# Kernel optimization log

Hardware: AMD Instinct MI355X
Metric: run time of the kernel (lower is better)

Reference implementation:

```python
import jax, jax.numpy as jnp
import numpy as np

S = 4096      # sequence length == contextlen
D_IN = 1024   # input_size
E = 512       # embed_dim = input_size // 2 (divisor=2)
OUT = 256     # output_size (action dim)
HEAD_DIM = 2  # E // num_heads, num_heads = input_size // 4 = 256


def _w(k, shape):
    return jax.random.normal(k, shape, dtype=jnp.float32) * 0.02


def setup_inputs() -> dict:
    key = jax.random.key(0)
    ks = jax.random.split(key, 12)
    return {
        "x": jax.random.normal(ks[0], (S, D_IN), dtype=jnp.float32),
        # Encoder: D_IN -> 2D -> 4D -> 2D -> E (torch Linear: y = x W^T + b)
        "enc_w1": _w(ks[1], (2 * D_IN, D_IN)), "enc_b1": jnp.zeros((2 * D_IN,), jnp.float32),
        "enc_w2": _w(ks[2], (4 * D_IN, 2 * D_IN)), "enc_b2": jnp.zeros((4 * D_IN,), jnp.float32),
        "enc_w3": _w(ks[3], (2 * D_IN, 4 * D_IN)), "enc_b3": jnp.zeros((2 * D_IN,), jnp.float32),
        "enc_w4": _w(ks[4], (E, 2 * D_IN)), "enc_b4": jnp.zeros((E,), jnp.float32),
        # MultiheadDiffAttention packed qkv + out projection + lambda
        "in_proj_w": _w(ks[5], (3 * E, E)), "in_proj_b": jnp.zeros((3 * E,), jnp.float32),
        "out_proj_w": _w(ks[6], (E, E)), "out_proj_b": jnp.zeros((E,), jnp.float32),
        "lam": jnp.float32(0.8),
        # Actor head: E -> D_IN -> 2D_IN -> OUT
        "act_w1": _w(ks[7], (D_IN, E)), "act_b1": jnp.zeros((D_IN,), jnp.float32),
        "act_w2": _w(ks[8], (2 * D_IN, D_IN)), "act_b2": jnp.zeros((2 * D_IN,), jnp.float32),
        "act_w3": _w(ks[9], (OUT, 2 * D_IN)), "act_b3": jnp.zeros((OUT,), jnp.float32),
    }


def _pos_encoding(seq_len, d):
    pos = jnp.arange(seq_len, dtype=jnp.float32)[:, None]
    div = jnp.exp(jnp.arange(0, d, 2, dtype=jnp.float32) * (-np.log(10000.0) / d))
    pe = jnp.zeros((seq_len, d), jnp.float32)
    pe = pe.at[:, 0::2].set(jnp.sin(pos * div))
    pe = pe.at[:, 1::2].set(jnp.cos(pos * div))
    return pe


def reference(x, enc_w1, enc_b1, enc_w2, enc_b2, enc_w3, enc_b3, enc_w4, enc_b4,
              in_proj_w, in_proj_b, out_proj_w, out_proj_b, lam,
              act_w1, act_b1, act_w2, act_b2, act_w3, act_b3):
    relu = jax.nn.relu
    # Encoder MLP
    h = relu(x @ enc_w1.T + enc_b1)
    h = relu(h @ enc_w2.T + enc_b2)
    h = relu(h @ enc_w3.T + enc_b3)
    h = h @ enc_w4.T + enc_b4                      # (S, E)
    # Positional add
    h = h + _pos_encoding(S, E)
    # Differential dual-softmax attention (unbatched, heads never split)
    qkv = h @ in_proj_w.T + in_proj_b              # (S, 3E)
    q, k, v = jnp.split(qkv, 3, axis=-1)
    q1, q2 = jnp.split(q, 2, axis=-1)              # (S, E/2) each
    k1, k2 = jnp.split(k, 2, axis=-1)
    scale = 1.0 / np.sqrt(HEAD_DIM)
    a1 = jax.nn.softmax(jnp.matmul(q1, k1.T) * scale, axis=-1)   # (S, S)
    a2 = jax.nn.softmax(jnp.matmul(q2, k2.T) * scale, axis=-1)   # (S, S)
    # faithful quirk: boolean triu mask is ADDED (as 0/1) post-softmax
    causal_add = jnp.triu(jnp.ones((S, S), jnp.float32), k=1)
    diff = a1 - lam * a2 + causal_add
    attn_out = jnp.matmul(diff, v)                 # (S, E)
    # faithful quirk: transpose(0,1) then row-major view(S, -1, E)
    attn_out = jnp.reshape(attn_out.T, (S, 1, E))
    attn_out = attn_out @ out_proj_w.T + out_proj_b
    h = attn_out[:, 0, :]                          # squeeze(1)
    # Actor head
    h = relu(h @ act_w1.T + act_b1)
    h = relu(h @ act_w2.T + act_b2)
    h = h @ act_w3.T + act_b3                      # (S, OUT)
    logits = h[-1]                                 # (OUT,)
    return jax.nn.softmax(logits, axis=0)
```

## Files before the change

### kernel.cpp

```cpp
#include <hip/hip_runtime.h>
#include <cstdint>
#include <cstddef>

typedef __bf16 bf16x8 __attribute__((ext_vector_type(8)));
typedef float  f32x4  __attribute__((ext_vector_type(4)));

#define LDS_AS __attribute__((address_space(3)))
#define GLB_AS __attribute__((address_space(1)))

static __device__ __forceinline__ unsigned short f2bf(float f) {
    unsigned int u = __float_as_uint(f);
    u += 0x7fffu + ((u >> 16) & 1u);
    return (unsigned short)(u >> 16);
}

__global__ __launch_bounds__(256) void cvt_f32_bf16(const float* __restrict__ in,
                                                    unsigned short* __restrict__ out, int n4) {
    int stride = gridDim.x * blockDim.x;
    for (int i = blockIdx.x * blockDim.x + threadIdx.x; i < n4; i += stride) {
        float4 f = reinterpret_cast<const float4*>(in)[i];
        ushort4 u;
        u.x = f2bf(f.x); u.y = f2bf(f.y); u.z = f2bf(f.z); u.w = f2bf(f.w);
        reinterpret_cast<ushort4*>(out)[i] = u;
    }
}

__global__ void divtab_kernel(float* __restrict__ dtab) {
    int i = threadIdx.x;
    dtab[i] = expf((float)(2 * i) * (-9.210340371976184f / 512.0f));
}

template<int EPI>
__global__ __launch_bounds__(512, 2) void gemm256_bt(
    const unsigned short* __restrict__ A, int lda,
    const unsigned short* __restrict__ B, int ldb,
    int M, int N, int K,
    const float* __restrict__ bias,
    unsigned short* __restrict__ Cb, int ldc)
{
    __shared__ __align__(16) unsigned short lds[4][2][8192];

    const int nbn = N >> 8;
    int wg = blockIdx.x;
    {
        int q = gridDim.x >> 3;
        wg = (wg & 7) * q + (wg >> 3);
    }
    const int bm = wg / nbn, bn = wg % nbn;

    const int t = threadIdx.x;
    const int lane = t & 63, wid = t >> 6;
    const int wr = wid >> 2, wc = wid & 3;
    const int l15 = lane & 15, l4 = lane >> 4;

    const int sr = t >> 2;
    const int ss = (t & 3) ^ ((sr >> 1) & 3);
    const unsigned short* gA0 = A + (size_t)(bm * 256 + sr      ) * lda + ss * 8;
    const unsigned short* gA1 = A + (size_t)(bm * 256 + sr + 128) * lda + ss * 8;
    const unsigned short* gB0 = B + (size_t)(bn * 256 + sr      ) * ldb + ss * 8;
    const unsigned short* gB1 = B + (size_t)(bn * 256 + sr + 128) * ldb + ss * 8;

    const int rsw  = ((l4 ^ ((l15 >> 1) & 3)) << 4);
    const int aoff = (wr * 128 + l15) * 64 + rsw;
    const int boff = (wc * 64  + l15) * 64 + rsw;

    f32x4 acc[8][4];
    const f32x4 z = {0.f, 0.f, 0.f, 0.f};
#pragma unroll
    for (int i = 0; i < 8; i++)
#pragma unroll
        for (int j = 0; j < 4; j++) acc[i][j] = z;

    const int nk = K >> 5;

#define STAGE_A(kt_) do { int b_ = (kt_) & 3;                                              \
        __builtin_amdgcn_global_load_lds((const GLB_AS void*)(gA0 + (kt_) * 32),           \
            (LDS_AS void*)&lds[b_][0][wid * 512], 16, 0, 0);                               \
        __builtin_amdgcn_global_load_lds((const GLB_AS void*)(gA1 + (kt_) * 32),           \
            (LDS_AS void*)&lds[b_][0][4096 + wid * 512], 16, 0, 0); } while (0)
#define STAGE_B(kt_) do { int b_ = (kt_) & 3;                                              \
        __builtin_amdgcn_global_load_lds((const GLB_AS void*)(gB0 + (kt_) * 32),           \
            (LDS_AS void*)&lds[b_][1][wid * 512], 16, 0, 0);                               \
        __builtin_amdgcn_global_load_lds((const GLB_AS void*)(gB1 + (kt_) * 32),           \
            (LDS_AS void*)&lds[b_][1][4096 + wid * 512], 16, 0, 0); } while (0)

    STAGE_A(0); STAGE_B(0);
    STAGE_A(1); STAGE_B(1);
    asm volatile("s_waitcnt vmcnt(4)" ::: "memory");
    __builtin_amdgcn_s_barrier();
    __builtin_amdgcn_sched_barrier(0);

    for (int kt = 0; kt < nk; ++kt) {
        const int b = kt & 3;
        const LDS_AS char* abase = (const LDS_AS char*)&lds[b][0][0] + aoff;
        const LDS_AS char* bbase = (const LDS_AS char*)&lds[b][1][0] + boff;

        bf16x8 af[4], bfr[4];
#pragma unroll
        for (int i = 0; i < 4; ++i) af[i]  = *(const LDS_AS bf16x8*)(abase + i * 1024);
#pragma unroll
        for (int j = 0; j < 4; ++j) bfr[j] = *(const LDS_AS bf16x8*)(bbase + j * 1024);
        if (kt + 2 < nk) STAGE_A(kt + 2);
        __builtin_amdgcn_s_barrier();
        asm volatile("s_waitcnt lgkmcnt(0)" ::: "memory");
        __builtin_amdgcn_sched_barrier(0);
        __builtin_amdgcn_s_setprio(1);
#pragma unroll
        for (int i = 0; i < 4; ++i)
#pragma unroll
            for (int j = 0; j < 4; ++j)
                acc[i][j] = __builtin_amdgcn_mfma_f32_16x16x32_bf16(af[i], bfr[j], acc[i][j], 0, 0, 0);
        __builtin_amdgcn_s_setprio(0);
        __builtin_amdgcn_sched_barrier(0);
        __builtin_amdgcn_s_barrier();

#pragma unroll
        for (int i = 0; i < 4; ++i) af[i] = *(const LDS_AS bf16x8*)(abase + 4096 + i * 1024);
        if (kt + 2 < nk) {
            STAGE_B(kt + 2);
            asm volatile("s_waitcnt vmcnt(4)" ::: "memory");
        } else {
            asm volatile("s_waitcnt vmcnt(0)" ::: "memory");
        }
        __builtin_amdgcn_s_barrier();
        asm volatile("s_waitcnt lgkmcnt(0)" ::: "memory");
        __builtin_amdgcn_sched_barrier(0);
        __builtin_amdgcn_s_setprio(1);
#pragma unroll
        for (int i = 0; i < 4; ++i)
#pragma unroll
            for (int j = 0; j < 4; ++j)
                acc[4 + i][j] = __builtin_amdgcn_mfma_f32_16x16x32_bf16(af[i], bfr[j], acc[4 + i][j], 0, 0, 0);
        __builtin_amdgcn_s_setprio(0);
        __builtin_amdgcn_sched_barrier(0);
        __builtin_amdgcn_s_barrier();
    }
#undef STAGE_A
#undef STAGE_B

    const int row0 = bm * 256 + wr * 128;
    const int col0 = bn * 256 + wc * 64;
#pragma unroll
    for (int mi = 0; mi < 8; mi++) {
#pragma unroll
        for (int ni = 0; ni < 4; ni++) {
            f32x4 c = acc[mi][ni];
            const int col = col0 + ni * 16 + l15;
            const float bv = bias[col];
#pragma unroll
            for (int r = 0; r < 4; r++) {
                const int row = row0 + mi * 16 + l4 * 4 + r;
                float v = c[r] + bv;
                if (EPI == 0) v = fmaxf(v, 0.f);
                Cb[(size_t)row * ldc + col] = f2bf(v);
            }
        }
    }
}

template<int EPI>
__global__ __launch_bounds__(256) void gemm_bt(
    const unsigned short* __restrict__ A, int lda,
    const unsigned short* __restrict__ B, int ldb,
    int M, int N, int K,
    const float* __restrict__ bias,
    unsigned short* __restrict__ Cb, float* __restrict__ Cf, int ldc,
    float scale, const float* __restrict__ dtab)
{
    __shared__ unsigned short ldsA[128 * 32];
    __shared__ unsigned short ldsB[128 * 32];

    const int nbn = N >> 7;
    const int bm = blockIdx.x / nbn, bn = blockIdx.x % nbn;
    const int t = threadIdx.x;
    const int lane = t & 63, wid = t >> 6;
    const int wr = wid >> 1, wc = wid & 1;
    const int l15 = lane & 15, l4 = lane >> 4;

    const unsigned short* ga0 = A + (size_t)(bm * 128 + (t >> 2)) * lda + (t & 3) * 8;
    const unsigned short* gb0 = B + (size_t)(bn * 128 + (t >> 2)) * ldb + (t & 3) * 8;
    const size_t a64 = (size_t)64 * lda, b64 = (size_t)64 * ldb;
    LDS_AS void* laD0 = (LDS_AS void*)(&ldsA[wid * 512]);
    LDS_AS void* laD1 = (LDS_AS void*)(&ldsA[2048 + wid * 512]);
    LDS_AS void* lbD0 = (LDS_AS void*)(&ldsB[wid * 512]);
    LDS_AS void* lbD1 = (LDS_AS void*)(&ldsB[2048 + wid * 512]);

    const bf16x8* pa = (const bf16x8*)&ldsA[(wr * 64 + l15) * 32 + l4 * 8];
    const bf16x8* pb = (const bf16x8*)&ldsB[(wc * 64 + l15) * 32 + l4 * 8];

    f32x4 acc[4][4];
    const f32x4 z = {0.f, 0.f, 0.f, 0.f};
#pragma unroll
    for (int i = 0; i < 4; i++)
#pragma unroll
        for (int j = 0; j < 4; j++) acc[i][j] = z;

    const int nk = K >> 5;
    for (int kt = 0; kt < nk; ++kt) {
        const unsigned short* ga = ga0 + kt * 32;
        const unsigned short* gb = gb0 + kt * 32;
        __builtin_amdgcn_global_load_lds((const GLB_AS void*)ga,         laD0, 16, 0, 0);
        __builtin_amdgcn_global_load_lds((const GLB_AS void*)(ga + a64), laD1, 16, 0, 0);
        __builtin_amdgcn_global_load_lds((const GLB_AS void*)gb,         lbD0, 16, 0, 0);
        __builtin_amdgcn_global_load_lds((const GLB_AS void*)(gb + b64), lbD1, 16, 0, 0);
        __syncthreads();

        bf16x8 af[4], bfr[4];
#pragma unroll
        for (int mi = 0; mi < 4; mi++) af[mi]  = pa[mi * 64];
#pragma unroll
        for (int ni = 0; ni < 4; ni++) bfr[ni] = pb[ni * 64];
#pragma unroll
        for (int mi = 0; mi < 4; mi++)
#pragma unroll
            for (int ni = 0; ni < 4; ni++)
                acc[mi][ni] = __builtin_amdgcn_mfma_f32_16x16x32_bf16(af[mi], bfr[ni], acc[mi][ni], 0, 0, 0);
        __syncthreads();
    }

    const int row0 = bm * 128 + wr * 64;
    const int col0 = bn * 128 + wc * 64;
#pragma unroll
    for (int mi = 0; mi < 4; mi++) {
#pragma unroll
        for (int ni = 0; ni < 4; ni++) {
            f32x4 c = acc[mi][ni];
            const int col = col0 + ni * 16 + l15;
            float bv = 0.f, dv = 0.f;
            if (EPI != 3) bv = bias[col];
            if (EPI == 2) dv = dtab[col >> 1];
#pragma unroll
            for (int r = 0; r < 4; r++) {
                const int row = row0 + mi * 16 + l4 * 4 + r;
                float v = c[r] + bv;
                if (EPI == 0) v = fmaxf(v, 0.f);
                if (EPI == 2) {
                    float ang = (float)row * dv;
                    v += (col & 1) ? cosf(ang) : sinf(ang);
                }
                if (EPI == 3) {
                    Cf[(size_t)row * ldc + col] = v * scale;
                } else {
                    Cb[(size_t)row * ldc + col] = f2bf(v);
                    if (EPI == 2) Cf[(size_t)row * ldc + col] = v;
                }
            }
        }
    }
}

__global__ __launch_bounds__(256) void vcol_kernel(const float* __restrict__ Hf,
                                                   const float* __restrict__ ipw,
                                                   const float* __restrict__ ipb,
                                                   float* __restrict__ v) {
    const int row = blockIdx.x * 4 + (threadIdx.x >> 6);
    const int lane = threadIdx.x & 63;
    const float* w = ipw + (size_t)1535 * 512;
    const float* h = Hf + (size_t)row * 512;
    float s = 0.f;
    for (int k = lane; k < 512; k += 64) s += h[k] * w[k];
#pragma unroll
    for (int off = 32; off; off >>= 1) s += __shfl_down(s, off);
    if (lane == 0) v[row] = s + ipb[1535];
}

__global__ __launch_bounds__(256) void attn_rows(const float* __restrict__ S1,
                                                 const float* __restrict__ S2,
                                                 const float* __restrict__ v,
                                                 const float* __restrict__ lamp,
                                                 float* __restrict__ out) {
    const int r = blockIdx.x;
    const int tid = threadIdx.x, lane = tid & 63, wid = tid >> 6;
    const float* s1 = S1 + (size_t)r * 4096;
    const float* s2 = S2 + (size_t)r * 4096;
    __shared__ float red[4][8];

    float m1 = -1e30f, m2 = -1e30f;
    for (int i = tid; i < 4096; i += 256) {
        m1 = fmaxf(m1, s1[i]);
        m2 = fmaxf(m2, s2[i]);
    }
#pragma unroll
    for (int off = 32; off; off >>= 1) {
        m1 = fmaxf(m1, __shfl_down(m1, off));
        m2 = fmaxf(m2, __shfl_down(m2, off));
    }
    if (lane == 0) { red[wid][0] = m1; red[wid][1] = m2; }
    __syncthreads();
    m1 = fmaxf(fmaxf(red[0][0], red[1][0]), fmaxf(red[2][0], red[3][0]));
    m2 = fmaxf(fmaxf(red[0][1], red[1][1]), fmaxf(red[2][1], red[3][1]));

    const int gj = 3584 + r;
    float e1 = 0.f, e2 = 0.f, d1 = 0.f, d2 = 0.f, cs = 0.f;
    for (int i = tid; i < 4096; i += 256) {
        float p1 = expf(s1[i] - m1);
        float p2 = expf(s2[i] - m2);
        float vv = v[i];
        e1 += p1; e2 += p2; d1 += p1 * vv; d2 += p2 * vv;
        if (i > gj) cs += vv;
    }
#pragma unroll
    for (int off = 32; off; off >>= 1) {
        e1 += __shfl_down(e1, off); e2 += __shfl_down(e2, off);
        d1 += __shfl_down(d1, off); d2 += __shfl_down(d2, off);
        cs += __shfl_down(cs, off);
    }
    __syncthreads();
    if (lane == 0) {
        red[wid][0] = e1; red[wid][1] = e2; red[wid][2] = d1; red[wid][3] = d2; red[wid][4] = cs;
    }
    __syncthreads();
    if (tid == 0) {
        e1 = red[0][0] + red[1][0] + red[2][0] + red[3][0];
        e2 = red[0][1] + red[1][1] + red[2][1] + red[3][1];
        d1 = red[0][2] + red[1][2] + red[2][2] + red[3][2];
        d2 = red[0][3] + red[1][3] + red[2][3] + red[3][3];
        cs = red[0][4] + red[1][4] + red[2][4] + red[3][4];
        out[r] = d1 / e1 - lamp[0] * (d2 / e2) + cs;
    }
}

template<int RELU>
__global__ __launch_bounds__(256) void matvec(const float* __restrict__ W, const float* __restrict__ x,
                                              const float* __restrict__ b, float* __restrict__ y,
                                              int N, int K) {
    const int o = blockIdx.x * 4 + (threadIdx.x >> 6);
    const int lane = threadIdx.x & 63;
    if (o >= N) return;
    const float* w = W + (size_t)o * K;
    float s = 0.f;
    for (int k = lane; k < K; k += 64) s += w[k] * x[k];
#pragma unroll
    for (int off = 32; off; off >>= 1) s += __shfl_down(s, off);
    if (lane == 0) y[o] = RELU ? fmaxf(s + b[o], 0.f) : (s + b[o]);
}

__global__ __launch_bounds__(256) void softmax256(const float* __restrict__ lg, float* __restrict__ out) {
    const int tid = threadIdx.x, lane = tid & 63, wid = tid >> 6;
    __shared__ float rm[4], rs[4];
    float l = lg[tid];
    float m = l;
#pragma unroll
    for (int off = 32; off; off >>= 1) m = fmaxf(m, __shfl_down(m, off));
    if (lane == 0) rm[wid] = m;
    __syncthreads();
    m = fmaxf(fmaxf(rm[0], rm[1]), fmaxf(rm[2], rm[3]));
    float e = expf(l - m);
    float s = e;
#pragma unroll
    for (int off = 32; off; off >>= 1) s += __shfl_down(s, off);
    if (lane == 0) rs[wid] = s;
    __syncthreads();
    s = rs[0] + rs[1] + rs[2] + rs[3];
    out[tid] = e / s;
}

extern "C" void kernel_launch(void* const* d_in, const int* in_sizes, int n_in,
                              void* d_out, int out_size, void* d_ws, size_t ws_size,
                              hipStream_t stream) {
    const float* x      = (const float*)d_in[0];
    const float* enc_w1 = (const float*)d_in[1];
    const float* enc_b1 = (const float*)d_in[2];
    const float* enc_w2 = (const float*)d_in[3];
    const float* enc_b2 = (const float*)d_in[4];
    const float* enc_w3 = (const float*)d_in[5];
    const float* enc_b3 = (const float*)d_in[6];
    const float* enc_w4 = (const float*)d_in[7];
    const float* enc_b4 = (const float*)d_in[8];
    const float* ipw    = (const float*)d_in[9];
    const float* ipb    = (const float*)d_in[10];
    const float* opw    = (const float*)d_in[11];
    const float* opb    = (const float*)d_in[12];
    const float* lam    = (const float*)d_in[13];
    const float* aw1    = (const float*)d_in[14];
    const float* ab1    = (const float*)d_in[15];
    const float* aw2    = (const float*)d_in[16];
    const float* ab2    = (const float*)d_in[17];
    const float* aw3    = (const float*)d_in[18];
    const float* ab3    = (const float*)d_in[19];

    char* ws = (char*)d_ws;
    const size_t MB = 1ull << 20;
    unsigned short* bufA = (unsigned short*)(ws);
    unsigned short* bufB = (unsigned short*)(ws + 32 * MB);
    float* S1            = (float*)(ws + 32 * MB);
    float* S2            = (float*)(ws + 40 * MB);
    unsigned short* Wb   = (unsigned short*)(ws + 48 * MB);
    unsigned short* IPb  = (unsigned short*)(ws + 64 * MB);
    unsigned short* Hb   = (unsigned short*)(ws + 66 * MB);
    float* Hf            = (float*)(ws + 70 * MB);
    unsigned short* Kb   = (unsigned short*)(ws + 78 * MB);
    unsigned short* Qb   = (unsigned short*)(ws + 82 * MB);
    float* vcol          = (float*)(ws + 83 * MB);
    float* dtab          = (float*)(ws + 83 * MB + 64 * 1024);
    float* attnv         = (float*)(ws + 83 * MB + 128 * 1024);
    float* hh            = (float*)(ws + 83 * MB + 192 * 1024);
    float* h1            = (float*)(ws + 83 * MB + 256 * 1024);
    float* h2            = (float*)(ws + 83 * MB + 320 * 1024);
    float* lg            = (float*)(ws + 83 * MB + 384 * 1024);

    auto cvt = [&](const float* in, unsigned short* outp, int n) {
        int n4 = n >> 2;
        int blocks = (n4 + 255) / 256;
        if (blocks > 2048) blocks = 2048;
        cvt_f32_bf16<<<dim3(blocks), dim3(256), 0, stream>>>(in, outp, n4);
    };

    divtab_kernel<<<dim3(1), dim3(256), 0, stream>>>(dtab);

    cvt(x, bufA, 4096 * 1024);
    cvt(enc_w1, Wb, 2048 * 1024);
    gemm256_bt<0><<<dim3(16 * 8), dim3(512), 0, stream>>>(bufA, 1024, Wb, 1024, 4096, 2048, 1024,
                                                          enc_b1, bufB, 2048);
    cvt(enc_w2, Wb, 4096 * 2048);
    gemm256_bt<0><<<dim3(16 * 16), dim3(512), 0, stream>>>(bufB, 2048, Wb, 2048, 4096, 4096, 2048,
                                                           enc_b2, bufA, 4096);
    cvt(enc_w3, Wb, 2048 * 4096);
    gemm256_bt<0><<<dim3(16 * 8), dim3(512), 0, stream>>>(bufA, 4096, Wb, 4096, 4096, 2048, 4096,
                                                          enc_b3, bufB, 2048);
    cvt(enc_w4, Wb, 512 * 2048);
    gemm_bt<2><<<dim3(32 * 4), dim3(256), 0, stream>>>(bufB, 2048, Wb, 2048, 4096, 512, 2048,
                                                       enc_b4, Hb, Hf, 512, 1.f, dtab);

    cvt(ipw, IPb, 1536 * 512);
    gemm_bt<1><<<dim3(32 * 4), dim3(256), 0, stream>>>(Hb, 512, IPb + 512 * 512, 512, 4096, 512, 512,
                                                       ipb + 512, Kb, nullptr, 512, 1.f, nullptr);
    gemm_bt<1><<<dim3(4 * 4), dim3(256), 0, stream>>>(Hb + (size_t)3584 * 512, 512, IPb, 512, 512, 512, 512,
                                                      ipb, Qb, nullptr, 512, 1.f, nullptr);
    vcol_kernel<<<dim3(1024), dim3(256), 0, stream>>>(Hf, ipw, ipb, vcol);

    const float rs2 = 0.70710678118654752f;
    gemm_bt<3><<<dim3(4 * 32), dim3(256), 0, stream>>>(Qb, 512, Kb, 512, 512, 4096, 256,
                                                       nullptr, nullptr, S1, 4096, rs2, nullptr);
    gemm_bt<3><<<dim3(4 * 32), dim3(256), 0, stream>>>(Qb + 256, 512, Kb + 256, 512, 512, 4096, 256,
                                                       nullptr, nullptr, S2, 4096, rs2, nullptr);

    attn_rows<<<dim3(512), dim3(256), 0, stream>>>(S1, S2, vcol, lam, attnv);

    matvec<0><<<dim3(128), dim3(256), 0, stream>>>(opw, attnv, opb, hh, 512, 512);
    matvec<1><<<dim3(256), dim3(256), 0, stream>>>(aw1, hh, ab1, h1, 1024, 512);
    matvec<1><<<dim3(512), dim3(256), 0, stream>>>(aw2, h1, ab2, h2, 2048, 1024);
    matvec<0><<<dim3(64), dim3(256), 0, stream>>>(aw3, h2, ab3, lg, 256, 2048);
    softmax256<<<dim3(1), dim3(256), 0, stream>>>(lg, (float*)d_out);
}
```

Measured before the change: 655.1 us.

## Template big GEMM on N tile width and deepen LDS prefetch to three stages

The 256x256 bf16 GEMM becomes a template on the N-tile width. The two 2048-wide encoder layers now use 256x128 tiles, doubling their workgroup count from 128 to 256 so all CUs on the device get work. The software pipeline also prefetches three K-steps ahead instead of two, with the vmcnt waits adjusted to match, to hide more global-load latency. The narrower tiles reuse each A element across fewer columns, which raises global traffic per FLOP for those layers.

```diff
diff --git a/kernel.cpp b/kernel.cpp
--- a/kernel.cpp
+++ b/kernel.cpp
@@ -1,6 +1,7 @@
 #include <hip/hip_runtime.h>
 #include <cstdint>
 #include <cstddef>
+
 
 typedef __bf16 bf16x8 __attribute__((ext_vector_type(8)));
 typedef float  f32x4  __attribute__((ext_vector_type(4)));
@@ -30,7 +31,7 @@
     dtab[i] = expf((float)(2 * i) * (-9.210340371976184f / 512.0f));
 }
 
-template<int EPI>
+template<int EPI, int NB, int ID>
 __global__ __launch_bounds__(512, 2) void gemm256_bt(
     const unsigned short* __restrict__ A, int lda,
     const unsigned short* __restrict__ B, int ldb,
@@ -38,9 +39,14 @@
     const float* __restrict__ bias,
     unsigned short* __restrict__ Cb, int ldc)
 {
-    __shared__ __align__(16) unsigned short lds[4][2][8192];
-
-    const int nbn = N >> 8;
+    constexpr int BROWS  = NB;
+    constexpr int NI     = NB / 64;
+    constexpr int WCROWS = NB / 4;
+    constexpr int SLOTSH = 256 * 32 + BROWS * 32;
+    constexpr int SLOTB  = SLOTSH * 2;
+    __shared__ __align__(16) unsigned short lds[4 * SLOTSH];
+
+    const int nbn = N / NB;
     int wg = blockIdx.x;
     {
         int q = gridDim.x >> 3;
@@ -55,52 +61,57 @@
 
     const int sr = t >> 2;
     const int ss = (t & 3) ^ ((sr >> 1) & 3);
-    const unsigned short* gA0 = A + (size_t)(bm * 256 + sr      ) * lda + ss * 8;
-    const unsigned short* gA1 = A + (size_t)(bm * 256 + sr + 128) * lda + ss * 8;
-    const unsigned short* gB0 = B + (size_t)(bn * 256 + sr      ) * ldb + ss * 8;
-    const unsigned short* gB1 = B + (size_t)(bn * 256 + sr + 128) * ldb + ss * 8;
+    const unsigned short* gA0 = A + (size_t)(bm * 256 + sr) * lda + ss * 8;
+    const unsigned short* gA1 = gA0 + (size_t)128 * lda;
+    const unsigned short* gB0 = B + (size_t)(bn * NB + sr) * ldb + ss * 8;
+    const unsigned short* gB1 = gB0 + (size_t)128 * ldb;
 
     const int rsw  = ((l4 ^ ((l15 >> 1) & 3)) << 4);
     const int aoff = (wr * 128 + l15) * 64 + rsw;
-    const int boff = (wc * 64  + l15) * 64 + rsw;
-
-    f32x4 acc[8][4];
+    const int boff = 16384 + (wc * WCROWS + l15) * 64 + rsw;
+
+    f32x4 acc[8][NI];
     const f32x4 z = {0.f, 0.f, 0.f, 0.f};
 #pragma unroll
     for (int i = 0; i < 8; i++)
 #pragma unroll
-        for (int j = 0; j < 4; j++) acc[i][j] = z;
+        for (int j = 0; j < NI; j++) acc[i][j] = z;
 
     const int nk = K >> 5;
 
-#define STAGE_A(kt_) do { int b_ = (kt_) & 3;                                              \
-        __builtin_amdgcn_global_load_lds((const GLB_AS void*)(gA0 + (kt_) * 32),           \
-            (LDS_AS void*)&lds[b_][0][wid * 512], 16, 0, 0);                               \
-        __builtin_amdgcn_global_load_lds((const GLB_AS void*)(gA1 + (kt_) * 32),           \
-            (LDS_AS void*)&lds[b_][0][4096 + wid * 512], 16, 0, 0); } while (0)
-#define STAGE_B(kt_) do { int b_ = (kt_) & 3;                                              \
-        __builtin_amdgcn_global_load_lds((const GLB_AS void*)(gB0 + (kt_) * 32),           \
-            (LDS_AS void*)&lds[b_][1][wid * 512], 16, 0, 0);                               \
-        __builtin_amdgcn_global_load_lds((const GLB_AS void*)(gB1 + (kt_) * 32),           \
-            (LDS_AS void*)&lds[b_][1][4096 + wid * 512], 16, 0, 0); } while (0)
+#define STAGE_A(kt_) do { int s_ = (kt_) & 3;                                              \
+        unsigned short* d_ = &lds[s_ * SLOTSH + t * 8];                                    \
+        __builtin_amdgcn_global_load_lds((const GLB_AS void*)(gA0 + (size_t)(kt_) * 32),   \
+                                         (LDS_AS void*)d_, 16, 0, 0);                      \
+        __builtin_amdgcn_global_load_lds((const GLB_AS void*)(gA1 + (size_t)(kt_) * 32),   \
+                                         (LDS_AS void*)(d_ + 4096), 16, 0, 0); } while (0)
+#define STAGE_B(kt_) do { int s_ = (kt_) & 3;                                              \
+        unsigned short* d_ = &lds[s_ * SLOTSH + 8192 + t * 8];                             \
+        __builtin_amdgcn_global_load_lds((const GLB_AS void*)(gB0 + (size_t)(kt_) * 32),   \
+                                         (LDS_AS void*)d_, 16, 0, 0);                      \
+        if (NB == 256)                                                                     \
+        __builtin_amdgcn_global_load_lds((const GLB_AS void*)(gB1 + (size_t)(kt_) * 32),   \
+                                         (LDS_AS void*)(d_ + 4096), 16, 0, 0); } while (0)
 
     STAGE_A(0); STAGE_B(0);
     STAGE_A(1); STAGE_B(1);
-    asm volatile("s_waitcnt vmcnt(4)" ::: "memory");
+    STAGE_A(2); STAGE_B(2);
+    if (NB == 256) asm volatile("s_waitcnt vmcnt(8)" ::: "memory");
+    else           asm volatile("s_waitcnt vmcnt(6)" ::: "memory");
     __builtin_amdgcn_s_barrier();
     __builtin_amdgcn_sched_barrier(0);
 
     for (int kt = 0; kt < nk; ++kt) {
-        const int b = kt & 3;
-        const LDS_AS char* abase = (const LDS_AS char*)&lds[b][0][0] + aoff;
-        const LDS_AS char* bbase = (const LDS_AS char*)&lds[b][1][0] + boff;
-
-        bf16x8 af[4], bfr[4];
-#pragma unroll
-        for (int i = 0; i < 4; ++i) af[i]  = *(const LDS_AS bf16x8*)(abase + i * 1024);
-#pragma unroll
-        for (int j = 0; j < 4; ++j) bfr[j] = *(const LDS_AS bf16x8*)(bbase + j * 1024);
-        if (kt + 2 < nk) STAGE_A(kt + 2);
+        const int s = kt & 3;
+        const LDS_AS char* ab = (const LDS_AS char*)&lds[0] + s * SLOTB + aoff;
+        const LDS_AS char* bb = (const LDS_AS char*)&lds[0] + s * SLOTB + boff;
+
+        bf16x8 af[4], bfr[NI];
+#pragma unroll
+        for (int i = 0; i < 4; ++i) af[i]  = *(const LDS_AS bf16x8*)(ab + i * 1024);
+#pragma unroll
+        for (int j = 0; j < NI; ++j) bfr[j] = *(const LDS_AS bf16x8*)(bb + j * 1024);
+        if (kt + 3 < nk) STAGE_A(kt + 3);
         __builtin_amdgcn_s_barrier();
         asm volatile("s_waitcnt lgkmcnt(0)" ::: "memory");
         __builtin_amdgcn_sched_barrier(0);
@@ -108,17 +119,18 @@
 #pragma unroll
         for (int i = 0; i < 4; ++i)
 #pragma unroll
-            for (int j = 0; j < 4; ++j)
+            for (int j = 0; j < NI; ++j)
                 acc[i][j] = __builtin_amdgcn_mfma_f32_16x16x32_bf16(af[i], bfr[j], acc[i][j], 0, 0, 0);
         __builtin_amdgcn_s_setprio(0);
         __builtin_amdgcn_sched_barrier(0);
         __builtin_amdgcn_s_barrier();
 
 #pragma unroll
-        for (int i = 0; i < 4; ++i) af[i] = *(const LDS_AS bf16x8*)(abase + 4096 + i * 1024);
-        if (kt + 2 < nk) {
-            STAGE_B(kt + 2);
-            asm volatile("s_waitcnt vmcnt(4)" ::: "memory");
+        for (int i = 0; i < 4; ++i) af[i] = *(const LDS_AS bf16x8*)(ab + 4096 + i * 1024);
+        if (kt + 3 < nk) {
+            STAGE_B(kt + 3);
+            if (NB == 256) asm volatile("s_waitcnt vmcnt(8)" ::: "memory");
+            else           asm volatile("s_waitcnt vmcnt(6)" ::: "memory");
         } else {
             asm volatile("s_waitcnt vmcnt(0)" ::: "memory");
         }
@@ -129,7 +141,7 @@
 #pragma unroll
         for (int i = 0; i < 4; ++i)
 #pragma unroll
-            for (int j = 0; j < 4; ++j)
+            for (int j = 0; j < NI; ++j)
                 acc[4 + i][j] = __builtin_amdgcn_mfma_f32_16x16x32_bf16(af[i], bfr[j], acc[4 + i][j], 0, 0, 0);
         __builtin_amdgcn_s_setprio(0);
         __builtin_amdgcn_sched_barrier(0);
@@ -139,11 +151,11 @@
 #undef STAGE_B
 
     const int row0 = bm * 256 + wr * 128;
-    const int col0 = bn * 256 + wc * 64;
+    const int col0 = bn * NB + wc * WCROWS;
 #pragma unroll
     for (int mi = 0; mi < 8; mi++) {
 #pragma unroll
-        for (int ni = 0; ni < 4; ni++) {
+        for (int ni = 0; ni < NI; ni++) {
             f32x4 c = acc[mi][ni];
             const int col = col0 + ni * 16 + l15;
             const float bv = bias[col];
@@ -410,14 +422,14 @@
 
     cvt(x, bufA, 4096 * 1024);
     cvt(enc_w1, Wb, 2048 * 1024);
-    gemm256_bt<0><<<dim3(16 * 8), dim3(512), 0, stream>>>(bufA, 1024, Wb, 1024, 4096, 2048, 1024,
-                                                          enc_b1, bufB, 2048);
+    gemm256_bt<0, 128, 1><<<dim3(16 * 16), dim3(512), 0, stream>>>(bufA, 1024, Wb, 1024,
+                                                                   4096, 2048, 1024, enc_b1, bufB, 2048);
     cvt(enc_w2, Wb, 4096 * 2048);
-    gemm256_bt<0><<<dim3(16 * 16), dim3(512), 0, stream>>>(bufB, 2048, Wb, 2048, 4096, 4096, 2048,
-                                                           enc_b2, bufA, 4096);
+    gemm256_bt<0, 256, 2><<<dim3(16 * 16), dim3(512), 0, stream>>>(bufB, 2048, Wb, 2048,
+                                                                   4096, 4096, 2048, enc_b2, bufA, 4096);
     cvt(enc_w3, Wb, 2048 * 4096);
-    gemm256_bt<0><<<dim3(16 * 8), dim3(512), 0, stream>>>(bufA, 4096, Wb, 4096, 4096, 2048, 4096,
-                                                          enc_b3, bufB, 2048);
+    gemm256_bt<0, 128, 3><<<dim3(16 * 16), dim3(512), 0, stream>>>(bufA, 4096, Wb, 4096,
+                                                                   4096, 2048, 4096, enc_b3, bufB, 2048);
     cvt(enc_w4, Wb, 512 * 2048);
     gemm_bt<2><<<dim3(32 * 4), dim3(256), 0, stream>>>(bufB, 2048, Wb, 2048, 4096, 512, 2048,
                                                        enc_b4, Hb, Hf, 512, 1.f, dtab);
```

Result: faster. 608.1 us (-7.2%).
